# Optimization experiments

Hardware: AMD Instinct MI355X
Metric: run time of the kernel (lower is better)

The kernel has to match this reference:

```python
import jax, jax.numpy as jnp
import numpy as np

F = 128   # flattened observation features
H = 64    # MLP/LSTM hidden size (hardcoded in module)
A = 15    # number of discrete actions
T = 128   # rollout length (timesteps)
B = 2048  # number of parallel envs (batch)


def setup_inputs() -> dict:
    key = jax.random.key(0)
    ks = jax.random.split(key, 12)
    n = lambda k, sh, s=1.0: jax.random.normal(k, sh, jnp.float32) * s
    return {
        "x": n(ks[0], (T * B, F)),
        "done": (jax.random.uniform(ks[1], (T * B,)) < 0.05).astype(jnp.float32),
        "h0": n(ks[2], (1, B, H)),
        "c0": n(ks[3], (1, B, H)),
        # MLP encoder params (Linear stores y = x @ W + b here, W: [in, out])
        "W1": n(ks[4], (F, H), 0.1), "b1": jnp.zeros((H,), jnp.float32),
        "W2": n(ks[5], (H, H), 0.1), "b2": jnp.zeros((H,), jnp.float32),
        # LSTM params, PyTorch layout: weight_ih [4H, H_in], gate order i,f,g,o
        "Wih": n(ks[6], (4 * H, H), 0.1), "bih": jnp.zeros((4 * H,), jnp.float32),
        "Whh": n(ks[7], (4 * H, H), 0.1), "bhh": jnp.zeros((4 * H,), jnp.float32),
        # actor / critic heads
        "Wa": n(ks[8], (H, A), 0.01), "ba": jnp.zeros((A,), jnp.float32),
        "Wc": n(ks[9], (H, 1), 1.0), "bc": jnp.zeros((1,), jnp.float32),
    }


def reference(x, done, h0, c0, W1, b1, W2, b2, Wih, bih, Whh, bhh, Wa, ba, Wc, bc):
    Bsz, Hh = h0.shape[1], h0.shape[2]
    # MLP encoder: Linear -> Tanh -> Linear -> Tanh
    y = jnp.tanh(x @ W1 + b1)
    y = jnp.tanh(y @ W2 + b2)                 # [T*B, H]
    y = y.reshape(-1, Bsz, Hh)                # [T, B, H]
    d = done.reshape(-1, Bsz)                 # [T, B]

    def step(carry, td):
        h, c = carry
        yt, dt = td
        m = (1.0 - dt)[:, None]               # done-mask hidden reset
        h = h * m
        c = c * m
        g = yt @ Wih.T + bih + h @ Whh.T + bhh  # [B, 4H]
        i, f, gg, o = jnp.split(g, 4, axis=-1)
        c = jax.nn.sigmoid(f) * c + jax.nn.sigmoid(i) * jnp.tanh(gg)
        h = jax.nn.sigmoid(o) * jnp.tanh(c)
        return (h, c), h

    (hT, cT), outs = jax.lax.scan(step, (h0[0], c0[0]), (y, d))
    z = outs.reshape(-1, Hh)                  # [T*B, H]
    logits = z @ Wa + ba                      # Categorical logits
    vf = z @ Wc + bc
    return logits, vf, hT[None], cT[None]
```

## Files before the change

### kernel.cpp

```cpp
#include <hip/hip_runtime.h>
#include <hip/hip_bf16.h>
#include <stdint.h>

typedef __bf16  bf16x8 __attribute__((ext_vector_type(8)));
typedef short   s16x8  __attribute__((ext_vector_type(8)));
typedef int     i32x4  __attribute__((ext_vector_type(4)));
typedef float   f32x4  __attribute__((ext_vector_type(4)));

union Frag { s16x8 s; bf16x8 b; i32x4 i; };

static __device__ __forceinline__ short f2bf(float f) {
    union { float f; unsigned u; } v; v.f = f;
    unsigned r = (v.u + 0x7FFFu + ((v.u >> 16) & 1u)) >> 16;
    return (short)r;
}
static __device__ __forceinline__ float bf2f(short s) {
    union { unsigned u; float f; } v; v.u = ((unsigned)(unsigned short)s) << 16;
    return v.f;
}
static __device__ __forceinline__ float fast_rcp(float x) { return __builtin_amdgcn_rcpf(x); }
static __device__ __forceinline__ float sigm(float x) { return fast_rcp(1.0f + __expf(-x)); }
static __device__ __forceinline__ float tanh_fast(float x) {
    float e = __expf(-2.0f * x);
    return (1.0f - e) * fast_rcp(1.0f + e);
}
static __device__ __forceinline__ f32x4 mfma16(bf16x8 a, bf16x8 b, f32x4 c) {
    return __builtin_amdgcn_mfma_f32_16x16x32_bf16(a, b, c, 0, 0, 0);
}

#define GLDS(gp, lp) __builtin_amdgcn_global_load_lds( \
    (const __attribute__((address_space(1))) void*)(gp), \
    (__attribute__((address_space(3))) void*)(lp), 16, 0, 0)

#define TT 128
#define BB 2048
#define HH 64
#define FF 128
#define AA 15
#define CH 32
#define LOGITS_OFF 0
#define VF_OFF   3932160
#define HT_OFF   4194304
#define CT_OFF   4325376


__global__ __launch_bounds__(256) void enc_kernel(
    const float* __restrict__ x, const float* __restrict__ W1, const float* __restrict__ b1,
    const float* __restrict__ W2, const float* __restrict__ b2, short* __restrict__ y_sw)
{
    __shared__ short w1t[64][136];
    __shared__ short w2t[64][72];
    __shared__ short c1buf[4][16][72];
    __shared__ short ybuf[4][16][72];

    const int tid  = threadIdx.x;
    const int lane = tid & 63;
    const int w    = tid >> 6;
    const int c    = lane & 15;
    const int q    = lane >> 4;

    for (int i = tid; i < 128*64; i += 256) { int k = i >> 6, n = i & 63; w1t[n][k] = f2bf(W1[i]); }
    for (int i = tid; i < 64*64;  i += 256) { int k = i >> 6, n = i & 63; w2t[n][k] = f2bf(W2[i]); }

    float b1v[4], b2v[4];
#pragma unroll
    for (int ct = 0; ct < 4; ++ct) { b1v[ct] = b1[16*ct + c]; b2v[ct] = b2[16*ct + c]; }
    __syncthreads();

    for (int it = 0; it < 4; ++it) {
        const int wt = it*4096 + blockIdx.x*4 + w;
        const int r0 = wt * 16;
        Frag af[4];
#pragma unroll
        for (int kf = 0; kf < 4; ++kf) {
            const float* xp = x + (size_t)(r0 + c)*FF + 32*kf + 8*q;
            f32x4 x0 = *(const f32x4*)xp;
            f32x4 x1 = *(const f32x4*)(xp + 4);
#pragma unroll
            for (int jj = 0; jj < 4; ++jj) { af[kf].s[jj] = f2bf(x0[jj]); af[kf].s[4+jj] = f2bf(x1[jj]); }
        }
        f32x4 acc[4];
#pragma unroll
        for (int ct = 0; ct < 4; ++ct) acc[ct] = (f32x4){b1v[ct], b1v[ct], b1v[ct], b1v[ct]};
#pragma unroll
        for (int kf = 0; kf < 4; ++kf)
#pragma unroll
            for (int ct = 0; ct < 4; ++ct) {
                Frag bf; bf.s = *(const s16x8*)&w1t[16*ct + c][32*kf + 8*q];
                acc[ct] = mfma16(af[kf].b, bf.b, acc[ct]);
            }
#pragma unroll
        for (int ct = 0; ct < 4; ++ct)
#pragma unroll
            for (int i = 0; i < 4; ++i)
                c1buf[w][4*q + i][16*ct + c] = f2bf(tanh_fast(acc[ct][i]));
        Frag a2[2];
#pragma unroll
        for (int kf = 0; kf < 2; ++kf) a2[kf].s = *(const s16x8*)&c1buf[w][c][32*kf + 8*q];
        f32x4 acc2[4];
#pragma unroll
        for (int ct = 0; ct < 4; ++ct) acc2[ct] = (f32x4){b2v[ct], b2v[ct], b2v[ct], b2v[ct]};
#pragma unroll
        for (int kf = 0; kf < 2; ++kf)
#pragma unroll
            for (int ct = 0; ct < 4; ++ct) {
                Frag bf; bf.s = *(const s16x8*)&w2t[16*ct + c][32*kf + 8*q];
                acc2[ct] = mfma16(a2[kf].b, bf.b, acc2[ct]);
            }
#pragma unroll
        for (int ct = 0; ct < 4; ++ct)
#pragma unroll
            for (int i = 0; i < 4; ++i)
                ybuf[w][4*q + i][16*ct + c] = f2bf(tanh_fast(acc2[ct][i]));
#pragma unroll
        for (int kf = 0; kf < 2; ++kf) {
            s16x8 yv = *(const s16x8*)&ybuf[w][c][32*kf + 8*q];
            *(s16x8*)(y_sw + (size_t)wt*1024 + kf*512 + lane*8) = yv;
        }
    }
}

__global__ __launch_bounds__(256, 1) void scan_kernel(
    const short* __restrict__ y_sw, const float* __restrict__ done,
    const float* __restrict__ h0, const float* __restrict__ c0,
    const float* __restrict__ Wih, const float* __restrict__ bih,
    const float* __restrict__ Whh, const float* __restrict__ bhh,
    const float* __restrict__ Wa, const float* __restrict__ ba,
    const float* __restrict__ Wc, const float* __restrict__ bc,
    float* __restrict__ out_logits, float* __restrict__ out_vf,
    float* __restrict__ hT_out, float* __restrict__ cT_out)
{
    __shared__ short ybuf[CH][1024];
    __shared__ float obuf[CH][16][16];
    __shared__ short hbuf[2][16][72];
    __shared__ float dbuf[TT][16];

    const int tid  = threadIdx.x;
    const int lane = tid & 63;
    const int w    = tid >> 6;
    const int c    = lane & 15;
    const int q    = lane >> 4;
    const int blk  = blockIdx.x;
    const int b0   = blk * 16;
    const int jcol = 16*w + c;

    Frag  wf[4][4];
    float biasv[4];
#pragma unroll
    for (int a = 0; a < 4; ++a) {
        const int col = 64*a + jcol;
        biasv[a] = bih[col] + bhh[col];
#pragma unroll
        for (int kf = 0; kf < 4; ++kf) {
            const float* wp = (kf < 2) ? (Wih + (size_t)col*HH + 32*kf + 8*q)
                                       : (Whh + (size_t)col*HH + 32*(kf-2) + 8*q);
            f32x4 w0 = *(const f32x4*)wp;
            f32x4 w1 = *(const f32x4*)(wp + 4);
#pragma unroll
            for (int jj = 0; jj < 4; ++jj) { wf[a][kf].s[jj] = f2bf(w0[jj]); wf[a][kf].s[4+jj] = f2bf(w1[jj]); }
        }
    }
    Frag hwf[2]; float hbv;
#pragma unroll
    for (int kf = 0; kf < 2; ++kf)
#pragma unroll
        for (int jj = 0; jj < 8; ++jj) {
            int k = 32*kf + 8*q + jj;
            hwf[kf].s[jj] = f2bf((c < 15) ? Wa[k*AA + c] : Wc[k]);
        }
    hbv = (c < 15) ? ba[c] : bc[0];

    float cst[4];
#pragma unroll
    for (int i = 0; i < 4; ++i) cst[i] = c0[(size_t)(b0 + 4*q + i)*HH + jcol];
    {
        int mm = tid & 15, j4 = tid >> 4;
        f32x4 hv = *(const f32x4*)(h0 + (size_t)(b0 + mm)*HH + 4*j4);
#pragma unroll
        for (int ii = 0; ii < 4; ++ii) hbuf[0][mm][4*j4 + ii] = f2bf(hv[ii]);
    }
#pragma unroll
    for (int i = 0; i < 2; ++i) {
        int j = w*2 + i;
        const float* gp = done + (size_t)(16*j + (lane >> 2))*BB + b0 + 4*(lane & 3);
        GLDS(gp, &dbuf[16*j][0]);
    }
#pragma unroll
    for (int i = 0; i < 16; ++i) {
        int idx = w*16 + i, ss = idx >> 1, hh = idx & 1;
        const short* gp = y_sw + ((size_t)ss*128 + blk)*1024 + hh*512 + lane*8;
        GLDS(gp, &ybuf[ss][hh*512]);
    }
    __builtin_amdgcn_s_waitcnt(0x0F70);
    __syncthreads();

    for (int t = 0; t < TT; ++t) {
        const int cur = t & 1, nxt = cur ^ 1, s = t & (CH-1);
        Frag hf0, hf1;
        hf0.s = *(const s16x8*)&hbuf[cur][c][8*q];
        hf1.s = *(const s16x8*)&hbuf[cur][c][32 + 8*q];
        if (t > 0 && ((t-1) & 3) == w) {
            f32x4 ha = (f32x4){hbv, hbv, hbv, hbv};
            ha = mfma16(hf0.b, hwf[0].b, ha);
            ha = mfma16(hf1.b, hwf[1].b, ha);
            const int slot = (t-1) & (CH-1);
#pragma unroll
            for (int i = 0; i < 4; ++i) obuf[slot][4*q + i][c] = ha[i];
        }
        if (s == 0 && t > 0) {
            __syncthreads();
#pragma unroll
            for (int i = 0; i < 16; ++i) {
                int idx = w*16 + i, ss = idx >> 1, hh = idx & 1;
                const short* gp = y_sw + ((size_t)(t + ss)*128 + blk)*1024 + hh*512 + lane*8;
                GLDS(gp, &ybuf[ss][hh*512]);
            }
#pragma unroll
            for (int rep = 0; rep < 2; ++rep) {
                int idx = rep*256 + tid, ss = idx >> 4, rr = idx & 15;
                size_t row = (size_t)(t - CH + ss)*BB + b0 + rr;
                const float* ob = &obuf[ss][rr][0];
                float* lp = out_logits + row*AA;
#pragma unroll
                for (int n = 0; n < 15; ++n) lp[n] = ob[n];
                out_vf[row] = ob[15];
            }
            __builtin_amdgcn_s_waitcnt(0x0F70);
            __syncthreads();
        }
        const float dmv = dbuf[t][c];
        const int msk = (dmv != 0.0f) ? 0 : -1;
        Frag h0m, h1m;
#pragma unroll
        for (int k = 0; k < 4; ++k) { h0m.i[k] = hf0.i[k] & msk; h1m.i[k] = hf1.i[k] & msk; }
        Frag yc0, yc1;
        yc0.s = *(const s16x8*)&ybuf[s][lane*8];
        yc1.s = *(const s16x8*)&ybuf[s][512 + lane*8];
        f32x4 acc[4];
#pragma unroll
        for (int a = 0; a < 4; ++a) {
            acc[a] = (f32x4){biasv[a], biasv[a], biasv[a], biasv[a]};
            acc[a] = mfma16(yc0.b, wf[a][0].b, acc[a]);
            acc[a] = mfma16(yc1.b, wf[a][1].b, acc[a]);
            acc[a] = mfma16(h0m.b, wf[a][2].b, acc[a]);
            acc[a] = mfma16(h1m.b, wf[a][3].b, acc[a]);
        }
        const f32x4 dcv = *(const f32x4*)&dbuf[t][4*q];
#pragma unroll
        for (int i = 0; i < 4; ++i) {
            float gi = acc[0][i], gf = acc[1][i], gg = acc[2][i], go = acc[3][i];
            float cm = (dcv[i] != 0.0f) ? 0.0f : cst[i];
            float cn = sigm(gf)*cm + sigm(gi)*tanh_fast(gg);
            cst[i] = cn;
            hbuf[nxt][4*q + i][jcol] = f2bf(sigm(go)*tanh_fast(cn));
        }
        __syncthreads();
    }
    {
        Frag hf0, hf1;
        hf0.s = *(const s16x8*)&hbuf[0][c][8*q];
        hf1.s = *(const s16x8*)&hbuf[0][c][32 + 8*q];
        if (((TT-1) & 3) == w) {
            f32x4 ha = (f32x4){hbv, hbv, hbv, hbv};
            ha = mfma16(hf0.b, hwf[0].b, ha);
            ha = mfma16(hf1.b, hwf[1].b, ha);
#pragma unroll
            for (int i = 0; i < 4; ++i) obuf[(TT-1) & (CH-1)][4*q + i][c] = ha[i];
        }
        __syncthreads();
#pragma unroll
        for (int rep = 0; rep < 2; ++rep) {
            int idx = rep*256 + tid, ss = idx >> 4, rr = idx & 15;
            size_t row = (size_t)(TT - CH + ss)*BB + b0 + rr;
            const float* ob = &obuf[ss][rr][0];
            float* lp = out_logits + row*AA;
#pragma unroll
            for (int n = 0; n < 15; ++n) lp[n] = ob[n];
            out_vf[row] = ob[15];
        }
        {
            int mm = tid & 15, j4 = tid >> 4;
            f32x4 hv;
#pragma unroll
            for (int ii = 0; ii < 4; ++ii) hv[ii] = bf2f(hbuf[0][mm][4*j4 + ii]);
            *(f32x4*)(hT_out + (size_t)(b0 + mm)*HH + 4*j4) = hv;
        }
#pragma unroll
        for (int i = 0; i < 4; ++i) cT_out[(size_t)(b0 + 4*q + i)*HH + jcol] = cst[i];
    }
}

extern "C" void kernel_launch(void* const* d_in, const int* in_sizes, int n_in,
                              void* d_out, int out_size, void* d_ws, size_t ws_size,
                              hipStream_t stream) {
    const float* x    = (const float*)d_in[0];
    const float* done = (const float*)d_in[1];
    const float* h0   = (const float*)d_in[2];
    const float* c0   = (const float*)d_in[3];
    const float* W1   = (const float*)d_in[4];
    const float* b1   = (const float*)d_in[5];
    const float* W2   = (const float*)d_in[6];
    const float* b2   = (const float*)d_in[7];
    const float* Wih  = (const float*)d_in[8];
    const float* bih  = (const float*)d_in[9];
    const float* Whh  = (const float*)d_in[10];
    const float* bhh  = (const float*)d_in[11];
    const float* Wa   = (const float*)d_in[12];
    const float* ba   = (const float*)d_in[13];
    const float* Wc   = (const float*)d_in[14];
    const float* bc   = (const float*)d_in[15];
    float* out = (float*)d_out;

    short* y_sw = (short*)d_ws;

    enc_kernel<<<1024, 256, 0, stream>>>(x, W1, b1, W2, b2, y_sw);
    scan_kernel<<<128, 256, 0, stream>>>(y_sw, done, h0, c0, Wih, bih, Whh, bhh,
                                         Wa, ba, Wc, bc,
                                         out + LOGITS_OFF, out + VF_OFF,
                                         out + HT_OFF, out + CT_OFF);
}
```

Before: 330.7 us.

## Split scan block into critical-path and helper waves for input-projection pipelining

The scan kernel grows to 512 threads. Four critical waves do only the recurrent h@Whh MFMAs and the LSTM cell update. Four helper waves precompute the next step's y@Wih+bias gates into a double-buffered LDS buffer, handle the actor/critic head and output stores, and stream y chunks of 8 steps with double buffering. The done-mask is folded into the end of each step, so the recurrence's serial chain is shortened at the cost of more LDS traffic, extra waves and a barrier every step. The helper's setup code also computes a redundant gate accumulation.

```diff
diff --git a/kernel.cpp b/kernel.cpp
--- a/kernel.cpp
+++ b/kernel.cpp
@@ -37,7 +37,7 @@
 #define HH 64
 #define FF 128
 #define AA 15
-#define CH 32
+#define CH 8
 #define LOGITS_OFF 0
 #define VF_OFF   3932160
 #define HT_OFF   4194304
@@ -120,7 +120,7 @@
     }
 }
 
-__global__ __launch_bounds__(256, 1) void scan_kernel(
+__global__ __launch_bounds__(512, 1) void scan_kernel(
     const short* __restrict__ y_sw, const float* __restrict__ done,
     const float* __restrict__ h0, const float* __restrict__ c0,
     const float* __restrict__ Wih, const float* __restrict__ bih,
@@ -130,10 +130,12 @@
     float* __restrict__ out_logits, float* __restrict__ out_vf,
     float* __restrict__ hT_out, float* __restrict__ cT_out)
 {
-    __shared__ short ybuf[CH][1024];
-    __shared__ float obuf[CH][16][16];
+    __shared__ short ybuf[2][CH][1024];
+    __shared__ float gybuf[2][4][4][256];
+    __shared__ float obuf[2][CH][16][16];
+    __shared__ short zbuf[2][16][72];
     __shared__ short hbuf[2][16][72];
-    __shared__ float dbuf[TT][16];
+    __shared__ float dbuf[TT+1][16];
 
     const int tid  = threadIdx.x;
     const int lane = tid & 63;
@@ -142,149 +144,208 @@
     const int q    = lane >> 4;
     const int blk  = blockIdx.x;
     const int b0   = blk * 16;
-    const int jcol = 16*w + c;
-
-    Frag  wf[4][4];
+    const bool crit = (w < 4);
+    const int hw   = w - 4;
+
+    Frag  wf[4][2];
     float biasv[4];
-#pragma unroll
-    for (int a = 0; a < 4; ++a) {
-        const int col = 64*a + jcol;
-        biasv[a] = bih[col] + bhh[col];
-#pragma unroll
-        for (int kf = 0; kf < 4; ++kf) {
-            const float* wp = (kf < 2) ? (Wih + (size_t)col*HH + 32*kf + 8*q)
-                                       : (Whh + (size_t)col*HH + 32*(kf-2) + 8*q);
-            f32x4 w0 = *(const f32x4*)wp;
-            f32x4 w1 = *(const f32x4*)(wp + 4);
-#pragma unroll
-            for (int jj = 0; jj < 4; ++jj) { wf[a][kf].s[jj] = f2bf(w0[jj]); wf[a][kf].s[4+jj] = f2bf(w1[jj]); }
-        }
-    }
-    Frag hwf[2]; float hbv;
-#pragma unroll
-    for (int kf = 0; kf < 2; ++kf)
-#pragma unroll
-        for (int jj = 0; jj < 8; ++jj) {
-            int k = 32*kf + 8*q + jj;
-            hwf[kf].s[jj] = f2bf((c < 15) ? Wa[k*AA + c] : Wc[k]);
-        }
-    hbv = (c < 15) ? ba[c] : bc[0];
-
+    Frag  hwf[2];
+    float hbv = 0.f;
     float cst[4];
-#pragma unroll
-    for (int i = 0; i < 4; ++i) cst[i] = c0[(size_t)(b0 + 4*q + i)*HH + jcol];
-    {
-        int mm = tid & 15, j4 = tid >> 4;
+
+    if (crit) {
+        const int jcol = 16*w + c;
+#pragma unroll
+        for (int a = 0; a < 4; ++a) {
+            const int col = 64*a + jcol;
+#pragma unroll
+            for (int kf = 0; kf < 2; ++kf) {
+                const float* wp = Whh + (size_t)col*HH + 32*kf + 8*q;
+                f32x4 w0 = *(const f32x4*)wp;
+                f32x4 w1 = *(const f32x4*)(wp + 4);
+#pragma unroll
+                for (int jj = 0; jj < 4; ++jj) { wf[a][kf].s[jj] = f2bf(w0[jj]); wf[a][kf].s[4+jj] = f2bf(w1[jj]); }
+            }
+        }
+    } else {
+        const int jcolh = 16*hw + c;
+#pragma unroll
+        for (int a = 0; a < 4; ++a) {
+            const int col = 64*a + jcolh;
+            biasv[a] = bih[col] + bhh[col];
+#pragma unroll
+            for (int kf = 0; kf < 2; ++kf) {
+                const float* wp = Wih + (size_t)col*HH + 32*kf + 8*q;
+                f32x4 w0 = *(const f32x4*)wp;
+                f32x4 w1 = *(const f32x4*)(wp + 4);
+#pragma unroll
+                for (int jj = 0; jj < 4; ++jj) { wf[a][kf].s[jj] = f2bf(w0[jj]); wf[a][kf].s[4+jj] = f2bf(w1[jj]); }
+            }
+        }
+#pragma unroll
+        for (int kf = 0; kf < 2; ++kf)
+#pragma unroll
+            for (int jj = 0; jj < 8; ++jj) {
+                int k = 32*kf + 8*q + jj;
+                hwf[kf].s[jj] = f2bf((c < 15) ? Wa[k*AA + c] : Wc[k]);
+            }
+        hbv = (c < 15) ? ba[c] : bc[0];
+#pragma unroll
+        for (int i = 0; i < 2; ++i) {
+            int j = hw*2 + i;
+            const float* gp = done + (size_t)(16*j + (lane >> 2))*BB + b0 + 4*(lane & 3);
+            GLDS(gp, &dbuf[16*j][0]);
+        }
+#pragma unroll
+        for (int i = 0; i < 4; ++i) {
+            int idx = hw*4 + i, ss = idx >> 1, half = idx & 1;
+            const short* gp = y_sw + ((size_t)ss*128 + blk)*1024 + half*512 + lane*8;
+            GLDS(gp, &ybuf[0][ss][half*512]);
+        }
+        __builtin_amdgcn_s_waitcnt(0x0F70);
+    }
+    if (tid < 16) dbuf[TT][tid] = 0.0f;
+    __syncthreads();
+
+    if (crit) {
+        const int jcol = 16*w + c;
+#pragma unroll
+        for (int i = 0; i < 4; ++i) {
+            float d0 = dbuf[0][4*q + i];
+            float cv = c0[(size_t)(b0 + 4*q + i)*HH + jcol];
+            cst[i] = (d0 != 0.0f) ? 0.0f : cv;
+        }
+        int mm = tid & 15, j4 = (tid >> 4) & 15;
+        float dm = dbuf[0][mm];
         f32x4 hv = *(const f32x4*)(h0 + (size_t)(b0 + mm)*HH + 4*j4);
 #pragma unroll
-        for (int ii = 0; ii < 4; ++ii) hbuf[0][mm][4*j4 + ii] = f2bf(hv[ii]);
-    }
-#pragma unroll
-    for (int i = 0; i < 2; ++i) {
-        int j = w*2 + i;
-        const float* gp = done + (size_t)(16*j + (lane >> 2))*BB + b0 + 4*(lane & 3);
-        GLDS(gp, &dbuf[16*j][0]);
-    }
-#pragma unroll
-    for (int i = 0; i < 16; ++i) {
-        int idx = w*16 + i, ss = idx >> 1, hh = idx & 1;
-        const short* gp = y_sw + ((size_t)ss*128 + blk)*1024 + hh*512 + lane*8;
-        GLDS(gp, &ybuf[ss][hh*512]);
-    }
-    __builtin_amdgcn_s_waitcnt(0x0F70);
+        for (int ii = 0; ii < 4; ++ii)
+            hbuf[0][mm][4*j4 + ii] = (dm != 0.0f) ? (short)0 : f2bf(hv[ii]);
+    } else {
+        Frag yc0, yc1;
+        yc0.s = *(const s16x8*)&ybuf[0][0][lane*8];
+        yc1.s = *(const s16x8*)&ybuf[0][0][512 + lane*8];
+#pragma unroll
+        for (int a = 0; a < 4; ++a) {
+            f32x4 g = (f32x4){biasv[a], biasv[a], biasv[a], biasv[a]};
+            g = mfma16(yc0.b, wf[0+a][0].b, g);
+            g = mfma16(yc1.b, wf[a][1].b, g);
+            f32x4 gg = (f32x4){biasv[a], biasv[a], biasv[a], biasv[a]};
+            gg = mfma16(yc0.b, wf[a][0].b, gg);
+            gg = mfma16(yc1.b, wf[a][1].b, gg);
+            *(f32x4*)&gybuf[0][hw][a][lane*4] = gg;
+        }
+    }
     __syncthreads();
 
     for (int t = 0; t < TT; ++t) {
-        const int cur = t & 1, nxt = cur ^ 1, s = t & (CH-1);
-        Frag hf0, hf1;
-        hf0.s = *(const s16x8*)&hbuf[cur][c][8*q];
-        hf1.s = *(const s16x8*)&hbuf[cur][c][32 + 8*q];
-        if (t > 0 && ((t-1) & 3) == w) {
-            f32x4 ha = (f32x4){hbv, hbv, hbv, hbv};
-            ha = mfma16(hf0.b, hwf[0].b, ha);
-            ha = mfma16(hf1.b, hwf[1].b, ha);
-            const int slot = (t-1) & (CH-1);
-#pragma unroll
-            for (int i = 0; i < 4; ++i) obuf[slot][4*q + i][c] = ha[i];
-        }
-        if (s == 0 && t > 0) {
-            __syncthreads();
-#pragma unroll
-            for (int i = 0; i < 16; ++i) {
-                int idx = w*16 + i, ss = idx >> 1, hh = idx & 1;
-                const short* gp = y_sw + ((size_t)(t + ss)*128 + blk)*1024 + hh*512 + lane*8;
-                GLDS(gp, &ybuf[ss][hh*512]);
-            }
-#pragma unroll
-            for (int rep = 0; rep < 2; ++rep) {
-                int idx = rep*256 + tid, ss = idx >> 4, rr = idx & 15;
-                size_t row = (size_t)(t - CH + ss)*BB + b0 + rr;
-                const float* ob = &obuf[ss][rr][0];
+        if (crit) {
+            const int jcol = 16*w + c;
+            const int cur = t & 1;
+            Frag hf0, hf1;
+            hf0.s = *(const s16x8*)&hbuf[cur][c][8*q];
+            hf1.s = *(const s16x8*)&hbuf[cur][c][32 + 8*q];
+            f32x4 acc[4];
+#pragma unroll
+            for (int a = 0; a < 4; ++a) acc[a] = *(const f32x4*)&gybuf[cur][w][a][lane*4];
+#pragma unroll
+            for (int a = 0; a < 4; ++a) {
+                acc[a] = mfma16(hf0.b, wf[a][0].b, acc[a]);
+                acc[a] = mfma16(hf1.b, wf[a][1].b, acc[a]);
+            }
+            const f32x4 dn = *(const f32x4*)&dbuf[t+1][4*q];
+#pragma unroll
+            for (int i = 0; i < 4; ++i) {
+                float gi = acc[0][i], gf = acc[1][i], gg = acc[2][i], go = acc[3][i];
+                float cn = sigm(gf)*cst[i] + sigm(gi)*tanh_fast(gg);
+                float h  = sigm(go)*tanh_fast(cn);
+                short zb = f2bf(h);
+                zbuf[cur][4*q + i][jcol] = zb;
+                const bool d = (dn[i] != 0.0f);
+                cst[i] = d ? 0.0f : cn;
+                hbuf[cur ^ 1][4*q + i][jcol] = d ? (short)0 : zb;
+            }
+        } else {
+            if ((t & 7) == 0 && t < 120) {
+                const int k = (t >> 3) + 1;
+#pragma unroll
+                for (int i = 0; i < 4; ++i) {
+                    int idx = hw*4 + i, ss = idx >> 1, half = idx & 1;
+                    const short* gp = y_sw + ((size_t)(8*k + ss)*128 + blk)*1024 + half*512 + lane*8;
+                    GLDS(gp, &ybuf[k & 1][ss][half*512]);
+                }
+            }
+            if ((t & 7) == 1 && t > 8 && w < 6) {
+                const int cc = (t >> 3) - 1;
+                const int idx = (w - 4)*64 + lane;
+                const int s = idx >> 4, r = idx & 15;
+                const size_t row = (size_t)(8*cc + s)*BB + b0 + r;
+                const float* ob = &obuf[cc & 1][s][r][0];
                 float* lp = out_logits + row*AA;
 #pragma unroll
                 for (int n = 0; n < 15; ++n) lp[n] = ob[n];
                 out_vf[row] = ob[15];
             }
-            __builtin_amdgcn_s_waitcnt(0x0F70);
-            __syncthreads();
-        }
-        const float dmv = dbuf[t][c];
-        const int msk = (dmv != 0.0f) ? 0 : -1;
-        Frag h0m, h1m;
-#pragma unroll
-        for (int k = 0; k < 4; ++k) { h0m.i[k] = hf0.i[k] & msk; h1m.i[k] = hf1.i[k] & msk; }
-        Frag yc0, yc1;
-        yc0.s = *(const s16x8*)&ybuf[s][lane*8];
-        yc1.s = *(const s16x8*)&ybuf[s][512 + lane*8];
-        f32x4 acc[4];
-#pragma unroll
-        for (int a = 0; a < 4; ++a) {
-            acc[a] = (f32x4){biasv[a], biasv[a], biasv[a], biasv[a]};
-            acc[a] = mfma16(yc0.b, wf[a][0].b, acc[a]);
-            acc[a] = mfma16(yc1.b, wf[a][1].b, acc[a]);
-            acc[a] = mfma16(h0m.b, wf[a][2].b, acc[a]);
-            acc[a] = mfma16(h1m.b, wf[a][3].b, acc[a]);
-        }
-        const f32x4 dcv = *(const f32x4*)&dbuf[t][4*q];
-#pragma unroll
-        for (int i = 0; i < 4; ++i) {
-            float gi = acc[0][i], gf = acc[1][i], gg = acc[2][i], go = acc[3][i];
-            float cm = (dcv[i] != 0.0f) ? 0.0f : cst[i];
-            float cn = sigm(gf)*cm + sigm(gi)*tanh_fast(gg);
-            cst[i] = cn;
-            hbuf[nxt][4*q + i][jcol] = f2bf(sigm(go)*tanh_fast(cn));
+            if (t >= 1 && w == 4 + ((t-1) & 3)) {
+                const int tp = t - 1;
+                Frag zf0, zf1;
+                zf0.s = *(const s16x8*)&zbuf[tp & 1][c][8*q];
+                zf1.s = *(const s16x8*)&zbuf[tp & 1][c][32 + 8*q];
+                f32x4 ha = (f32x4){hbv, hbv, hbv, hbv};
+                ha = mfma16(zf0.b, hwf[0].b, ha);
+                ha = mfma16(zf1.b, hwf[1].b, ha);
+#pragma unroll
+                for (int i = 0; i < 4; ++i)
+                    obuf[(tp >> 3) & 1][tp & 7][4*q + i][c] = ha[i];
+            }
+            if (t < TT-1) {
+                const int tn = t + 1;
+                const int ch = (tn >> 3) & 1, sl = tn & 7;
+                Frag yc0, yc1;
+                yc0.s = *(const s16x8*)&ybuf[ch][sl][lane*8];
+                yc1.s = *(const s16x8*)&ybuf[ch][sl][512 + lane*8];
+#pragma unroll
+                for (int a = 0; a < 4; ++a) {
+                    f32x4 g = (f32x4){biasv[a], biasv[a], biasv[a], biasv[a]};
+                    g = mfma16(yc0.b, wf[a][0].b, g);
+                    g = mfma16(yc1.b, wf[a][1].b, g);
+                    *(f32x4*)&gybuf[tn & 1][hw][a][lane*4] = g;
+                }
+            }
+            if ((t & 7) == 6)
+                __builtin_amdgcn_s_waitcnt(0x0F70);
         }
         __syncthreads();
     }
-    {
-        Frag hf0, hf1;
-        hf0.s = *(const s16x8*)&hbuf[0][c][8*q];
-        hf1.s = *(const s16x8*)&hbuf[0][c][32 + 8*q];
-        if (((TT-1) & 3) == w) {
-            f32x4 ha = (f32x4){hbv, hbv, hbv, hbv};
-            ha = mfma16(hf0.b, hwf[0].b, ha);
-            ha = mfma16(hf1.b, hwf[1].b, ha);
-#pragma unroll
-            for (int i = 0; i < 4; ++i) obuf[(TT-1) & (CH-1)][4*q + i][c] = ha[i];
-        }
-        __syncthreads();
-#pragma unroll
-        for (int rep = 0; rep < 2; ++rep) {
-            int idx = rep*256 + tid, ss = idx >> 4, rr = idx & 15;
-            size_t row = (size_t)(TT - CH + ss)*BB + b0 + rr;
-            const float* ob = &obuf[ss][rr][0];
-            float* lp = out_logits + row*AA;
-#pragma unroll
-            for (int n = 0; n < 15; ++n) lp[n] = ob[n];
-            out_vf[row] = ob[15];
-        }
-        {
-            int mm = tid & 15, j4 = tid >> 4;
-            f32x4 hv;
-#pragma unroll
-            for (int ii = 0; ii < 4; ++ii) hv[ii] = bf2f(hbuf[0][mm][4*j4 + ii]);
-            *(f32x4*)(hT_out + (size_t)(b0 + mm)*HH + 4*j4) = hv;
-        }
+
+    if (!crit && w == 7) {
+        Frag zf0, zf1;
+        zf0.s = *(const s16x8*)&zbuf[1][c][8*q];
+        zf1.s = *(const s16x8*)&zbuf[1][c][32 + 8*q];
+        f32x4 ha = (f32x4){hbv, hbv, hbv, hbv};
+        ha = mfma16(zf0.b, hwf[0].b, ha);
+        ha = mfma16(zf1.b, hwf[1].b, ha);
+#pragma unroll
+        for (int i = 0; i < 4; ++i) obuf[1][7][4*q + i][c] = ha[i];
+    }
+    __syncthreads();
+    if (!crit && w < 6) {
+        const int idx = (w - 4)*64 + lane;
+        const int s = idx >> 4, r = idx & 15;
+        const size_t row = (size_t)(120 + s)*BB + b0 + r;
+        const float* ob = &obuf[1][s][r][0];
+        float* lp = out_logits + row*AA;
+#pragma unroll
+        for (int n = 0; n < 15; ++n) lp[n] = ob[n];
+        out_vf[row] = ob[15];
+    }
+    if (crit) {
+        const int jcol = 16*w + c;
+        int mm = tid & 15, j4 = (tid >> 4) & 15;
+        f32x4 hv;
+#pragma unroll
+        for (int ii = 0; ii < 4; ++ii) hv[ii] = bf2f(zbuf[1][mm][4*j4 + ii]);
+        *(f32x4*)(hT_out + (size_t)(b0 + mm)*HH + 4*j4) = hv;
 #pragma unroll
         for (int i = 0; i < 4; ++i) cT_out[(size_t)(b0 + 4*q + i)*HH + jcol] = cst[i];
     }
@@ -314,7 +375,7 @@
     short* y_sw = (short*)d_ws;
 
     enc_kernel<<<1024, 256, 0, stream>>>(x, W1, b1, W2, b2, y_sw);
-    scan_kernel<<<128, 256, 0, stream>>>(y_sw, done, h0, c0, Wih, bih, Whh, bhh,
+    scan_kernel<<<128, 512, 0, stream>>>(y_sw, done, h0, c0, Wih, bih, Whh, bhh,
                                          Wa, ba, Wc, bc,
                                          out + LOGITS_OFF, out + VF_OFF,
                                          out + HT_OFF, out + CT_OFF);
```

Result: faster. 319.6 us (-3.4%).

## Stream y prefetch per step and drain outputs incrementally in LSTM scan

Applied to the files above, without the earlier changes.

Reworks the scan loop so that y slices are prefetched one timestep at a time into a 32-slot ring, with one wave issuing each prefetch. The old design stalled every 32 steps on a bulk reload and an output flush behind two full barriers. Head outputs are now double-buffered in 8-step chunks and written out by half the lanes every 8 steps, and the per-step barrier waits only on LDS traffic, not on global loads. The MFMA operands are transposed so each lane holds 4 consecutive hidden columns, which allows vectorized h stores, c/h state loads, and bias loads. The cost is finer-grained issue logic and reliance on inline-asm barriers that never wait on vmcnt inside the loop.

```diff
diff --git a/kernel.cpp b/kernel.cpp
--- a/kernel.cpp
+++ b/kernel.cpp
@@ -4,6 +4,7 @@
 
 typedef __bf16  bf16x8 __attribute__((ext_vector_type(8)));
 typedef short   s16x8  __attribute__((ext_vector_type(8)));
+typedef short   s16x4  __attribute__((ext_vector_type(4)));
 typedef int     i32x4  __attribute__((ext_vector_type(4)));
 typedef float   f32x4  __attribute__((ext_vector_type(4)));
 
@@ -32,12 +33,15 @@
     (const __attribute__((address_space(1))) void*)(gp), \
     (__attribute__((address_space(3))) void*)(lp), 16, 0, 0)
 
+#define BAR_LGKM() asm volatile("s_waitcnt lgkmcnt(0)\n\ts_barrier" ::: "memory")
+#define BAR_ALL()  asm volatile("s_waitcnt vmcnt(0) lgkmcnt(0)\n\ts_barrier" ::: "memory")
+
 #define TT 128
 #define BB 2048
 #define HH 64
 #define FF 128
 #define AA 15
-#define CH 32
+#define YR 32
 #define LOGITS_OFF 0
 #define VF_OFF   3932160
 #define HT_OFF   4194304
@@ -130,10 +134,10 @@
     float* __restrict__ out_logits, float* __restrict__ out_vf,
     float* __restrict__ hT_out, float* __restrict__ cT_out)
 {
-    __shared__ short ybuf[CH][1024];
-    __shared__ float obuf[CH][16][16];
-    __shared__ short hbuf[2][16][72];
+    __shared__ short ybig[YR][1024];
+    __shared__ short zbuf[2][16][72];
     __shared__ float dbuf[TT][16];
+    __shared__ float obuf[2][8][16][16];
 
     const int tid  = threadIdx.x;
     const int lane = tid & 63;
@@ -142,25 +146,28 @@
     const int q    = lane >> 4;
     const int blk  = blockIdx.x;
     const int b0   = blk * 16;
-    const int jcol = 16*w + c;
-
-    Frag  wf[4][4];
-    float biasv[4];
+
+    Frag  wfr[4][4];
+    f32x4 biasv[4];
 #pragma unroll
     for (int a = 0; a < 4; ++a) {
-        const int col = 64*a + jcol;
-        biasv[a] = bih[col] + bhh[col];
+        const int gc = 64*a + 16*w + c;
 #pragma unroll
         for (int kf = 0; kf < 4; ++kf) {
-            const float* wp = (kf < 2) ? (Wih + (size_t)col*HH + 32*kf + 8*q)
-                                       : (Whh + (size_t)col*HH + 32*(kf-2) + 8*q);
+            const float* wp = (kf < 2) ? (Wih + (size_t)gc*HH + 32*kf + 8*q)
+                                       : (Whh + (size_t)gc*HH + 32*(kf-2) + 8*q);
             f32x4 w0 = *(const f32x4*)wp;
             f32x4 w1 = *(const f32x4*)(wp + 4);
 #pragma unroll
-            for (int jj = 0; jj < 4; ++jj) { wf[a][kf].s[jj] = f2bf(w0[jj]); wf[a][kf].s[4+jj] = f2bf(w1[jj]); }
-        }
-    }
-    Frag hwf[2]; float hbv;
+            for (int jj = 0; jj < 4; ++jj) { wfr[a][kf].s[jj] = f2bf(w0[jj]); wfr[a][kf].s[4+jj] = f2bf(w1[jj]); }
+        }
+        const int bcol = 64*a + 16*w + 4*q;
+        biasv[a] = *(const f32x4*)(bih + bcol);
+        f32x4 b2 = *(const f32x4*)(bhh + bcol);
+#pragma unroll
+        for (int jj = 0; jj < 4; ++jj) biasv[a][jj] += b2[jj];
+    }
+    Frag hwf[2];
 #pragma unroll
     for (int kf = 0; kf < 2; ++kf)
 #pragma unroll
@@ -168,16 +175,17 @@
             int k = 32*kf + 8*q + jj;
             hwf[kf].s[jj] = f2bf((c < 15) ? Wa[k*AA + c] : Wc[k]);
         }
-    hbv = (c < 15) ? ba[c] : bc[0];
-
-    float cst[4];
-#pragma unroll
-    for (int i = 0; i < 4; ++i) cst[i] = c0[(size_t)(b0 + 4*q + i)*HH + jcol];
+    const float hbv = (c < 15) ? ba[c] : bc[0];
+
+    f32x4 cst = *(const f32x4*)(c0 + (size_t)(b0 + c)*HH + 16*w + 4*q);
+
     {
-        int mm = tid & 15, j4 = tid >> 4;
-        f32x4 hv = *(const f32x4*)(h0 + (size_t)(b0 + mm)*HH + 4*j4);
-#pragma unroll
-        for (int ii = 0; ii < 4; ++ii) hbuf[0][mm][4*j4 + ii] = f2bf(hv[ii]);
+        int r = tid & 15, c4 = (tid >> 4) * 4;
+        f32x4 hv = *(const f32x4*)(h0 + (size_t)(b0 + r)*HH + c4);
+        s16x4 hp;
+#pragma unroll
+        for (int ii = 0; ii < 4; ++ii) hp[ii] = f2bf(hv[ii]);
+        *(s16x4*)&zbuf[1][r][c4] = hp;
     }
 #pragma unroll
     for (int i = 0; i < 2; ++i) {
@@ -185,109 +193,112 @@
         const float* gp = done + (size_t)(16*j + (lane >> 2))*BB + b0 + 4*(lane & 3);
         GLDS(gp, &dbuf[16*j][0]);
     }
-#pragma unroll
-    for (int i = 0; i < 16; ++i) {
-        int idx = w*16 + i, ss = idx >> 1, hh = idx & 1;
-        const short* gp = y_sw + ((size_t)ss*128 + blk)*1024 + hh*512 + lane*8;
-        GLDS(gp, &ybuf[ss][hh*512]);
-    }
-    __builtin_amdgcn_s_waitcnt(0x0F70);
-    __syncthreads();
+    for (int s = w; s < 31; s += 4)
+#pragma unroll
+        for (int half = 0; half < 2; ++half) {
+            const short* gp = y_sw + ((size_t)s*128 + blk)*1024 + half*512 + lane*8;
+            GLDS(gp, &ybig[s][half*512]);
+        }
+    BAR_ALL();
+
+    f32x4 hv;
 
     for (int t = 0; t < TT; ++t) {
-        const int cur = t & 1, nxt = cur ^ 1, s = t & (CH-1);
-        Frag hf0, hf1;
-        hf0.s = *(const s16x8*)&hbuf[cur][c][8*q];
-        hf1.s = *(const s16x8*)&hbuf[cur][c][32 + 8*q];
-        if (t > 0 && ((t-1) & 3) == w) {
+        const int rb = (t + 1) & 1, wb = t & 1, slot = t & (YR-1);
+        Frag z0, z1, y0, y1;
+        z0.s = *(const s16x8*)&zbuf[rb][c][8*q];
+        z1.s = *(const s16x8*)&zbuf[rb][c][32 + 8*q];
+        y0.s = *(const s16x8*)&ybig[slot][lane*8];
+        y1.s = *(const s16x8*)&ybig[slot][512 + lane*8];
+        const float dme = dbuf[t][c];
+        if (w == (t & 3) && t <= TT-32) {
+            const int ds = (t + 31) & (YR-1);
+#pragma unroll
+            for (int half = 0; half < 2; ++half) {
+                const short* gp = y_sw + ((size_t)(t+31)*128 + blk)*1024 + half*512 + lane*8;
+                GLDS(gp, &ybig[ds][half*512]);
+            }
+        }
+        if (t > 0 && w == (t & 3)) {
             f32x4 ha = (f32x4){hbv, hbv, hbv, hbv};
-            ha = mfma16(hf0.b, hwf[0].b, ha);
-            ha = mfma16(hf1.b, hwf[1].b, ha);
-            const int slot = (t-1) & (CH-1);
-#pragma unroll
-            for (int i = 0; i < 4; ++i) obuf[slot][4*q + i][c] = ha[i];
-        }
-        if (s == 0 && t > 0) {
-            __syncthreads();
-#pragma unroll
-            for (int i = 0; i < 16; ++i) {
-                int idx = w*16 + i, ss = idx >> 1, hh = idx & 1;
-                const short* gp = y_sw + ((size_t)(t + ss)*128 + blk)*1024 + hh*512 + lane*8;
-                GLDS(gp, &ybuf[ss][hh*512]);
-            }
-#pragma unroll
-            for (int rep = 0; rep < 2; ++rep) {
-                int idx = rep*256 + tid, ss = idx >> 4, rr = idx & 15;
-                size_t row = (size_t)(t - CH + ss)*BB + b0 + rr;
-                const float* ob = &obuf[ss][rr][0];
-                float* lp = out_logits + row*AA;
-#pragma unroll
-                for (int n = 0; n < 15; ++n) lp[n] = ob[n];
-                out_vf[row] = ob[15];
-            }
-            __builtin_amdgcn_s_waitcnt(0x0F70);
-            __syncthreads();
-        }
-        const float dmv = dbuf[t][c];
-        const int msk = (dmv != 0.0f) ? 0 : -1;
-        Frag h0m, h1m;
-#pragma unroll
-        for (int k = 0; k < 4; ++k) { h0m.i[k] = hf0.i[k] & msk; h1m.i[k] = hf1.i[k] & msk; }
-        Frag yc0, yc1;
-        yc0.s = *(const s16x8*)&ybuf[s][lane*8];
-        yc1.s = *(const s16x8*)&ybuf[s][512 + lane*8];
+            ha = mfma16(z0.b, hwf[0].b, ha);
+            ha = mfma16(z1.b, hwf[1].b, ha);
+            const int tp = t - 1;
+#pragma unroll
+            for (int i = 0; i < 4; ++i)
+                obuf[(tp >> 3) & 1][tp & 7][4*q + i][c] = ha[i];
+        }
+        const int msk = (dme != 0.0f) ? 0 : -1;
+        Frag zm0, zm1;
+#pragma unroll
+        for (int k = 0; k < 4; ++k) { zm0.i[k] = z0.i[k] & msk; zm1.i[k] = z1.i[k] & msk; }
         f32x4 acc[4];
 #pragma unroll
         for (int a = 0; a < 4; ++a) {
-            acc[a] = (f32x4){biasv[a], biasv[a], biasv[a], biasv[a]};
-            acc[a] = mfma16(yc0.b, wf[a][0].b, acc[a]);
-            acc[a] = mfma16(yc1.b, wf[a][1].b, acc[a]);
-            acc[a] = mfma16(h0m.b, wf[a][2].b, acc[a]);
-            acc[a] = mfma16(h1m.b, wf[a][3].b, acc[a]);
-        }
-        const f32x4 dcv = *(const f32x4*)&dbuf[t][4*q];
+            acc[a] = biasv[a];
+            acc[a] = mfma16(wfr[a][0].b, y0.b,  acc[a]);
+            acc[a] = mfma16(wfr[a][1].b, y1.b,  acc[a]);
+            acc[a] = mfma16(wfr[a][2].b, zm0.b, acc[a]);
+            acc[a] = mfma16(wfr[a][3].b, zm1.b, acc[a]);
+        }
 #pragma unroll
         for (int i = 0; i < 4; ++i) {
-            float gi = acc[0][i], gf = acc[1][i], gg = acc[2][i], go = acc[3][i];
-            float cm = (dcv[i] != 0.0f) ? 0.0f : cst[i];
-            float cn = sigm(gf)*cm + sigm(gi)*tanh_fast(gg);
+            float cm = (dme != 0.0f) ? 0.0f : cst[i];
+            float cn = sigm(acc[1][i])*cm + sigm(acc[0][i])*tanh_fast(acc[2][i]);
             cst[i] = cn;
-            hbuf[nxt][4*q + i][jcol] = f2bf(sigm(go)*tanh_fast(cn));
-        }
-        __syncthreads();
-    }
-    {
-        Frag hf0, hf1;
-        hf0.s = *(const s16x8*)&hbuf[0][c][8*q];
-        hf1.s = *(const s16x8*)&hbuf[0][c][32 + 8*q];
-        if (((TT-1) & 3) == w) {
-            f32x4 ha = (f32x4){hbv, hbv, hbv, hbv};
-            ha = mfma16(hf0.b, hwf[0].b, ha);
-            ha = mfma16(hf1.b, hwf[1].b, ha);
-#pragma unroll
-            for (int i = 0; i < 4; ++i) obuf[(TT-1) & (CH-1)][4*q + i][c] = ha[i];
-        }
-        __syncthreads();
-#pragma unroll
-        for (int rep = 0; rep < 2; ++rep) {
-            int idx = rep*256 + tid, ss = idx >> 4, rr = idx & 15;
-            size_t row = (size_t)(TT - CH + ss)*BB + b0 + rr;
-            const float* ob = &obuf[ss][rr][0];
+            hv[i]  = sigm(acc[3][i])*tanh_fast(cn);
+        }
+        {
+            s16x4 hp;
+#pragma unroll
+            for (int ii = 0; ii < 4; ++ii) hp[ii] = f2bf(hv[ii]);
+            *(s16x4*)&zbuf[wb][c][16*w + 4*q] = hp;
+        }
+        if ((t & 7) == 1 && t > 8 && lane < 32) {
+            const int cc = (t >> 3) - 1;
+            const int idx = w*32 + lane;
+            const int s = idx >> 4, r = idx & 15;
+            const float* ob = &obuf[cc & 1][s][r][0];
+            f32x4 o0 = *(const f32x4*)ob,     o1 = *(const f32x4*)(ob+4);
+            f32x4 o2 = *(const f32x4*)(ob+8), o3 = *(const f32x4*)(ob+12);
+            const size_t row = (size_t)(8*cc + s)*BB + b0 + r;
             float* lp = out_logits + row*AA;
-#pragma unroll
-            for (int n = 0; n < 15; ++n) lp[n] = ob[n];
-            out_vf[row] = ob[15];
-        }
-        {
-            int mm = tid & 15, j4 = tid >> 4;
-            f32x4 hv;
-#pragma unroll
-            for (int ii = 0; ii < 4; ++ii) hv[ii] = bf2f(hbuf[0][mm][4*j4 + ii]);
-            *(f32x4*)(hT_out + (size_t)(b0 + mm)*HH + 4*j4) = hv;
-        }
-#pragma unroll
-        for (int i = 0; i < 4; ++i) cT_out[(size_t)(b0 + 4*q + i)*HH + jcol] = cst[i];
-    }
+            lp[0]=o0[0]; lp[1]=o0[1]; lp[2]=o0[2]; lp[3]=o0[3];
+            lp[4]=o1[0]; lp[5]=o1[1]; lp[6]=o1[2]; lp[7]=o1[3];
+            lp[8]=o2[0]; lp[9]=o2[1]; lp[10]=o2[2]; lp[11]=o2[3];
+            lp[12]=o3[0]; lp[13]=o3[1]; lp[14]=o3[2];
+            out_vf[row] = o3[3];
+        }
+        BAR_LGKM();
+    }
+
+    if (w == 3) {
+        Frag z0, z1;
+        z0.s = *(const s16x8*)&zbuf[1][c][8*q];
+        z1.s = *(const s16x8*)&zbuf[1][c][32 + 8*q];
+        f32x4 ha = (f32x4){hbv, hbv, hbv, hbv};
+        ha = mfma16(z0.b, hwf[0].b, ha);
+        ha = mfma16(z1.b, hwf[1].b, ha);
+#pragma unroll
+        for (int i = 0; i < 4; ++i) obuf[1][7][4*q + i][c] = ha[i];
+    }
+    BAR_LGKM();
+    if (lane < 32) {
+        const int idx = w*32 + lane;
+        const int s = idx >> 4, r = idx & 15;
+        const float* ob = &obuf[1][s][r][0];
+        f32x4 o0 = *(const f32x4*)ob,     o1 = *(const f32x4*)(ob+4);
+        f32x4 o2 = *(const f32x4*)(ob+8), o3 = *(const f32x4*)(ob+12);
+        const size_t row = (size_t)(120 + s)*BB + b0 + r;
+        float* lp = out_logits + row*AA;
+        lp[0]=o0[0]; lp[1]=o0[1]; lp[2]=o0[2]; lp[3]=o0[3];
+        lp[4]=o1[0]; lp[5]=o1[1]; lp[6]=o1[2]; lp[7]=o1[3];
+        lp[8]=o2[0]; lp[9]=o2[1]; lp[10]=o2[2]; lp[11]=o2[3];
+        lp[12]=o3[0]; lp[13]=o3[1]; lp[14]=o3[2];
+        out_vf[row] = o3[3];
+    }
+    *(f32x4*)(hT_out + (size_t)(b0 + c)*HH + 16*w + 4*q) = hv;
+    *(f32x4*)(cT_out + (size_t)(b0 + c)*HH + 16*w + 4*q) = cst;
 }
 
 extern "C" void kernel_launch(void* const* d_in, const int* in_sizes, int n_in,
```

After: 326.7 us. No clear change (-1.2%).
